# Optimization experiments

Measured on AMD Instinct MI355X. Metric: run time of the kernel, lower is better.

Reference implementation:

```python
import jax, jax.numpy as jnp
import numpy as np

NUM_EMB = 8192
DIM = 64
DECAY = 0.99
EPS = 1e-05
COMMIT = 0.25


def setup_inputs() -> dict:
    key = jax.random.key(0)
    k1, k2, k3 = jax.random.split(key, 3)
    inputs = jax.random.normal(k1, (8, 4096, DIM), jnp.float32)
    weight = jax.random.normal(k2, (NUM_EMB, DIM), jnp.float32)
    ema_cluster_count = jnp.ones((NUM_EMB,), jnp.float32)
    ema_weight_sum = jax.random.normal(k3, (NUM_EMB, DIM), jnp.float32)
    return {
        'inputs': inputs,
        'weight': weight,
        'ema_cluster_count': ema_cluster_count,
        'ema_weight_sum': ema_weight_sum,
    }


def reference(inputs, weight, ema_cluster_count, ema_weight_sum):
    flat = inputs.reshape(-1, DIM)  # [N, D]
    distances = (
        jnp.sum(flat ** 2, axis=1, keepdims=True)
        + jnp.sum(weight ** 2, axis=1)
        - 2.0 * flat @ weight.T
    )
    idx = jnp.argmin(distances, axis=1)  # [N] int

    # EMA stats (training branch): one-hot column sums == segment counts,
    # encodings.T @ flat == segment sums of inputs by code index.
    counts = jax.ops.segment_sum(
        jnp.ones(flat.shape[0], jnp.float32), idx, num_segments=NUM_EMB)
    new_cc = ema_cluster_count * DECAY + (1.0 - DECAY) * counts
    emb_sum = jax.ops.segment_sum(flat, idx, num_segments=NUM_EMB)
    new_ws = ema_weight_sum * DECAY + (1.0 - DECAY) * emb_sum

    n = jnp.sum(new_cc)
    smoothed = (new_cc + EPS) / (n + NUM_EMB * EPS) * n
    new_weight = new_ws / smoothed[:, None]  # updated codebook [K, D]

    quantized_raw = new_weight[idx].reshape(inputs.shape)
    e_latent_loss = jnp.mean((jax.lax.stop_gradient(quantized_raw) - inputs) ** 2)
    vq_loss = COMMIT * e_latent_loss

    avg_probs = counts / flat.shape[0]
    perplexity = jnp.exp(-jnp.sum(avg_probs * jnp.log(avg_probs + 1e-10)))

    # straight-through estimator
    quantized = inputs + jax.lax.stop_gradient(quantized_raw - inputs)
    return quantized, vq_loss, idx, perplexity, new_weight, new_cc, new_ws
```

## Files before the change

### kernel.cpp

```cpp
#include <hip/hip_runtime.h>
#include <math.h>

typedef _Float16 f16x8 __attribute__((ext_vector_type(8)));
typedef float f32x4 __attribute__((ext_vector_type(4)));

#define NROWS 32768
#define KEMB  8192

#define DECAYF 0.99f
#define OMDF   0.01f

#define OUT_Q    0
#define OUT_LOSS 2097152
#define OUT_IDX  2097153
#define OUT_PERP 2129921
#define OUT_NW   2129922
#define OUT_NCC  2654210
#define OUT_NWS  2662402

#define WS_N      0
#define WS_ENT    1
#define WS_COUNTS 4
#define WS_EMB    8196
#define WS_IDX    532484
#define WS_W2H    565252
#define WS_WFRAG  573444
#define WS_ZERO_UNITS 532484

__device__ __forceinline__ float sq_rn(float v) { return __fmul_rn(v, v); }

__device__ __forceinline__ float npsumsq64(const float* vbuf) {
  float a[8];
#pragma unroll
  for (int j = 0; j < 8; ++j) a[j] = sq_rn(vbuf[j]);
#pragma unroll
  for (int m = 1; m < 8; ++m)
#pragma unroll
    for (int j = 0; j < 8; ++j) a[j] = __fadd_rn(a[j], sq_rn(vbuf[m*8 + j]));
  return __fadd_rn(__fadd_rn(__fadd_rn(a[0],a[1]), __fadd_rn(a[2],a[3])),
                   __fadd_rn(__fadd_rn(a[4],a[5]), __fadd_rn(a[6],a[7])));
}

__device__ __forceinline__ void split_f16(float x, _Float16& hi, _Float16& lo) {
  hi = (_Float16)x;
  float r = __fsub_rn(x, (float)hi);
  lo = (_Float16)r;
}

__global__ __launch_bounds__(256) void prep_kernel(const float* __restrict__ wg,
                                                   float* __restrict__ ws) {
  const int tid = blockIdx.x * 256 + threadIdx.x;
  if (tid < KEMB) {
    const float* src = wg + (size_t)tid * 64;
    float vbuf[64];
#pragma unroll
    for (int f = 0; f < 16; ++f) {
      float4 v = *(const float4*)(src + f*4);
      vbuf[f*4+0]=v.x; vbuf[f*4+1]=v.y; vbuf[f*4+2]=v.z; vbuf[f*4+3]=v.w;
    }
    ws[WS_W2H + tid] = __fmul_rn(0.5f, npsumsq64(vbuf));
  } else if (tid < KEMB + 65536) {
    const int u = tid - KEMB;
    const int K = u >> 3, g = u & 7;
    const int n = K & 15, P = K >> 4;
    const int slot = (g&3)*16 + n, shi = g >> 2;
    const float* src = wg + (size_t)K*64 + g*8;
    float4 v0 = *(const float4*)src, v1 = *(const float4*)(src + 4);
    float vv[8] = {v0.x,v0.y,v0.z,v0.w,v1.x,v1.y,v1.z,v1.w};
    f16x8 hi, lo;
#pragma unroll
    for (int j = 0; j < 8; ++j) { _Float16 h, l; split_f16(vv[j], h, l); hi[j]=h; lo[j]=l; }
    _Float16* wf = (_Float16*)(ws + WS_WFRAG);
    *(f16x8*)&wf[((size_t)(P*4 + shi)*64 + slot)*8]     = hi;
    *(f16x8*)&wf[((size_t)(P*4 + 2 + shi)*64 + slot)*8] = lo;
  }
}

#define COMPUTE_PANEL(I, B0, B1, B2, B3, W2)                                        \
  {                                                                                 \
    const f32x4 cin = {(W2), (W2), (W2), (W2)};                                     \
    f32x4 acc[4];                                                                   \
    _Pragma("unroll")                                                               \
    for (int rt = 0; rt < 4; ++rt) acc[rt] = __builtin_amdgcn_mfma_f32_16x16x32_f16(a[rt][0], (B0), cin, 0,0,0); \
    _Pragma("unroll")                                                               \
    for (int rt = 0; rt < 4; ++rt) acc[rt] = __builtin_amdgcn_mfma_f32_16x16x32_f16(a[rt][1], (B1), acc[rt], 0,0,0); \
    _Pragma("unroll")                                                               \
    for (int rt = 0; rt < 4; ++rt) acc[rt] = __builtin_amdgcn_mfma_f32_16x16x32_f16(a[rt][2], (B0), acc[rt], 0,0,0); \
    _Pragma("unroll")                                                               \
    for (int rt = 0; rt < 4; ++rt) acc[rt] = __builtin_amdgcn_mfma_f32_16x16x32_f16(a[rt][3], (B1), acc[rt], 0,0,0); \
    _Pragma("unroll")                                                               \
    for (int rt = 0; rt < 4; ++rt) acc[rt] = __builtin_amdgcn_mfma_f32_16x16x32_f16(a[rt][0], (B2), acc[rt], 0,0,0); \
    _Pragma("unroll")                                                               \
    for (int rt = 0; rt < 4; ++rt) acc[rt] = __builtin_amdgcn_mfma_f32_16x16x32_f16(a[rt][1], (B3), acc[rt], 0,0,0); \
    const int kk = (I)*64 + cg*16 + n16;                                            \
    _Pragma("unroll")                                                               \
    for (int rt = 0; rt < 4; ++rt)                                                  \
      _Pragma("unroll")                                                             \
      for (int reg = 0; reg < 4; ++reg) {                                           \
        const float dist = acc[rt][reg];                                            \
        const int bi = rt*4 + reg;                                                  \
        if (dist < best[bi]) { best[bi] = dist; bestk[bi] = kk; }                   \
      }                                                                             \
  }

#define LOADB(I, C0, C1, C2, C3, CW)                                                \
  {                                                                                 \
    const size_t base = ((size_t)((I)*4 + cg) * 256) * 8 + lane8;                   \
    C0 = *(const f16x8*)&wfrag[base];                                               \
    C1 = *(const f16x8*)&wfrag[base + 512];                                         \
    C2 = *(const f16x8*)&wfrag[base + 1024];                                        \
    C3 = *(const f16x8*)&wfrag[base + 1536];                                        \
    CW = w2hg[(I)*64 + cg*16 + n16];                                                \
  }

__global__ __launch_bounds__(512) void argmin_kernel(const float* __restrict__ xg,
                                                     float* __restrict__ out,
                                                     float* __restrict__ ws) {
  __shared__ __align__(16) _Float16 xp[8*4*64*8];
  __shared__ float md[128*4];
  __shared__ int   mk[128*4];
  __shared__ int   bkL[128];

  const int t    = threadIdx.x;
  const int lane = t & 63, wv = t >> 6;
  const int quad = lane >> 4, n16 = lane & 15;
  const int rg = wv >> 2, cg = wv & 3;
  const int row0 = blockIdx.x * 128;
  const _Float16* __restrict__ wfrag = (const _Float16*)(ws + WS_WFRAG);
  const float* __restrict__ w2hg = ws + WS_W2H;

#pragma unroll
  for (int it = 0; it < 2; ++it) {
    const int u  = t + 512*it;
    const int rp = u >> 7, n = (u >> 3) & 15, g = u & 7;
    const float* src = xg + (size_t)(row0 + rp*16 + n)*64 + g*8;
    float4 v0 = *(const float4*)src, v1 = *(const float4*)(src + 4);
    float vv[8] = {v0.x,v0.y,v0.z,v0.w,v1.x,v1.y,v1.z,v1.w};
    f16x8 hi, lo;
#pragma unroll
    for (int j = 0; j < 8; ++j) { _Float16 h, l; split_f16(-vv[j], h, l); hi[j]=h; lo[j]=l; }
    const int slot = (g&3)*16 + n, shi = g >> 2;
    *(f16x8*)&xp[(((rp*4) + shi)*64 + slot)*8]     = hi;
    *(f16x8*)&xp[(((rp*4) + 2 + shi)*64 + slot)*8] = lo;
  }
  __syncthreads();

  f16x8 a[4][4];
#pragma unroll
  for (int rt = 0; rt < 4; ++rt)
#pragma unroll
    for (int s = 0; s < 4; ++s)
      a[rt][s] = *(const f16x8*)&xp[(((rg*4+rt)*4 + s)*64 + lane)*8];

  float best[16]; int bestk[16];
#pragma unroll
  for (int i = 0; i < 16; ++i) { best[i] = INFINITY; bestk[i] = 0; }

  const size_t lane8 = (size_t)lane * 8;
  f16x8 p0, p1, p2, p3, q0, q1, q2, q3;
  float pw, qw;
  LOADB(0, p0, p1, p2, p3, pw);

  for (int it = 0; it < 128; it += 2) {
    LOADB(it+1, q0, q1, q2, q3, qw);
    COMPUTE_PANEL(it, p0, p1, p2, p3, pw);
    if (it + 2 < 128) LOADB(it+2, p0, p1, p2, p3, pw);
    COMPUTE_PANEL(it+1, q0, q1, q2, q3, qw);
  }

#pragma unroll
  for (int bi = 0; bi < 16; ++bi) {
    float bd = best[bi]; int bk = bestk[bi];
#pragma unroll
    for (int m = 1; m < 16; m <<= 1) {
      const float od = __shfl_xor(bd, m, 64);
      const int   ok = __shfl_xor(bk, m, 64);
      if (od < bd || (od == bd && ok < bk)) { bd = od; bk = ok; }
    }
    best[bi] = bd; bestk[bi] = bk;
  }
  if (n16 == 0) {
#pragma unroll
    for (int rt = 0; rt < 4; ++rt)
#pragma unroll
      for (int reg = 0; reg < 4; ++reg) {
        const int row = rg*64 + rt*16 + quad*4 + reg;
        md[row*4 + cg] = best[rt*4+reg];
        mk[row*4 + cg] = bestk[rt*4+reg];
      }
  }
  __syncthreads();

  if (t < 128) {
    const int row = t;
    float bd = md[row*4]; int bk = mk[row*4];
#pragma unroll
    for (int u = 1; u < 4; ++u) {
      const float d2 = md[row*4 + u]; const int k2 = mk[row*4 + u];
      if (d2 < bd || (d2 == bd && k2 < bk)) { bd = d2; bk = k2; }
    }
    out[OUT_IDX + row0 + row] = (float)bk;
    ((int*)ws)[WS_IDX + row0 + row] = bk;
    bkL[row] = bk;
    atomicAdd(&ws[WS_COUNTS + bk], 1.0f);
  }
  __syncthreads();

#pragma unroll 4
  for (int r = 0; r < 16; ++r) {
    const int row = wv*16 + r;
    const int k = bkL[row];
    atomicAdd(&ws[WS_EMB + (size_t)k*64 + lane],
              xg[(size_t)(row0 + row)*64 + lane]);
  }
}

__global__ __launch_bounds__(256) void stats_kernel(const float* __restrict__ cc,
                                                    float* __restrict__ out,
                                                    float* __restrict__ ws) {
  const int t = threadIdx.x;
  float v1 = 0.0f, v2 = 0.0f;
#pragma unroll
  for (int i = 0; i < 32; ++i) {
    const int k = i*256 + t;
    const float cnt = ws[WS_COUNTS + k];
    const float ncc = __fadd_rn(__fmul_rn(DECAYF, cc[k]), __fmul_rn(OMDF, cnt));
    out[OUT_NCC + k] = ncc;
    const float p = cnt * (1.0f/32768.0f);
    v1 += ncc;
    v2 += __fmul_rn(p, logf(__fadd_rn(p, 1e-10f)));
  }
#pragma unroll
  for (int off = 32; off > 0; off >>= 1) {
    v1 += __shfl_down(v1, off);
    v2 += __shfl_down(v2, off);
  }
  __shared__ float s1[4], s2[4];
  const int lane = t & 63, wid = t >> 6;
  if (lane == 0) { s1[wid] = v1; s2[wid] = v2; }
  __syncthreads();
  if (t == 0) {
    ws[WS_N]   = (s1[0]+s1[1]) + (s1[2]+s1[3]);
    ws[WS_ENT] = (s2[0]+s2[1]) + (s2[2]+s2[3]);
  }
}

__global__ __launch_bounds__(256) void update_kernel(const float* __restrict__ ws0,
                                                     float* __restrict__ out,
                                                     float* __restrict__ ws) {
  const int e4 = blockIdx.x * 256 + threadIdx.x;
  const int k = e4 >> 4;
  const float n = ws[WS_N];
  const float ncc = out[OUT_NCC + k];
  const float smoothed = __fmul_rn(__fadd_rn(ncc, 1e-5f) / __fadd_rn(n, 0.08192f), n);
  const float inv_s = 1.0f / smoothed;
  float4 w0 = *(const float4*)(ws0 + (size_t)e4*4);
  float4 em = *(const float4*)(ws + WS_EMB + (size_t)e4*4);
  float wv[4] = {w0.x, w0.y, w0.z, w0.w};
  float ev[4] = {em.x, em.y, em.z, em.w};
  float nwsv[4], nwv[4];
#pragma unroll
  for (int i = 0; i < 4; ++i) {
    nwsv[i] = __fadd_rn(__fmul_rn(DECAYF, wv[i]), __fmul_rn(OMDF, ev[i]));
    nwv[i]  = nwsv[i] / smoothed;
  }
  (void)inv_s;
  float4 onws = {nwsv[0], nwsv[1], nwsv[2], nwsv[3]};
  float4 onw  = {nwv[0],  nwv[1],  nwv[2],  nwv[3]};
  *(float4*)(out + OUT_NWS + (size_t)e4*4) = onws;
  *(float4*)(out + OUT_NW  + (size_t)e4*4) = onw;
  if (e4 == 0) out[OUT_PERP] = expf(-ws[WS_ENT]);
}

__global__ __launch_bounds__(256) void quant_kernel(const float* __restrict__ xg,
                                                    float* __restrict__ out,
                                                    float* __restrict__ ws) {
  const int t = threadIdx.x;
  const int* idxb = (const int*)ws + WS_IDX;
  float v = 0.0f;
#pragma unroll
  for (int j = 0; j < 4; ++j) {
    const int e4 = (j*512 + blockIdx.x)*256 + t;
    const int row = e4 >> 4, d = (e4 & 15) * 4;
    const int k = idxb[row];
    const float* nw = out + OUT_NW + (size_t)k*64 + d;
    float2 q0 = *(const float2*)nw, q1 = *(const float2*)(nw + 2);
    float4 x = *(const float4*)(xg + (size_t)e4*4);
    float qv[4] = {q0.x, q0.y, q1.x, q1.y};
    float xv[4] = {x.x, x.y, x.z, x.w};
    float4 o;
    float ov[4];
#pragma unroll
    for (int i = 0; i < 4; ++i) {
      const float df = __fsub_rn(qv[i], xv[i]);
      ov[i] = __fadd_rn(xv[i], df);
      v = fmaf(df, df, v);
    }
    o.x = ov[0]; o.y = ov[1]; o.z = ov[2]; o.w = ov[3];
    *(float4*)(out + OUT_Q + (size_t)e4*4) = o;
  }
#pragma unroll
  for (int off = 32; off > 0; off >>= 1) v += __shfl_down(v, off);
  __shared__ float sm[4];
  const int lane = t & 63, wid = t >> 6;
  if (lane == 0) sm[wid] = v;
  __syncthreads();
  if (t == 0) ws[WS_COUNTS + blockIdx.x] = (sm[0]+sm[1]) + (sm[2]+sm[3]);
}

__global__ void final_kernel(float* __restrict__ out, const float* __restrict__ ws) {
  const int t = threadIdx.x;
  float v = 0.0f;
#pragma unroll
  for (int i = 0; i < 8; ++i) v += ws[WS_COUNTS + i*64 + t];
#pragma unroll
  for (int off = 32; off > 0; off >>= 1) v += __shfl_down(v, off);
  if (t == 0) out[OUT_LOSS] = __fmul_rn(0.25f, v / 2097152.0f);
}

extern "C" void kernel_launch(void* const* d_in, const int* in_sizes, int n_in,
                              void* d_out, int out_size, void* d_ws, size_t ws_size,
                              hipStream_t stream) {
  (void)in_sizes; (void)n_in; (void)out_size; (void)ws_size;
  const float* x   = (const float*)d_in[0];
  const float* w   = (const float*)d_in[1];
  const float* cc  = (const float*)d_in[2];
  const float* ws0 = (const float*)d_in[3];
  float* out = (float*)d_out;
  float* ws  = (float*)d_ws;

  hipMemsetAsync(d_ws, 0, (size_t)WS_ZERO_UNITS * 4, stream);
  hipLaunchKernelGGL(prep_kernel,   dim3(288),  dim3(256), 0, stream, w, ws);
  hipLaunchKernelGGL(argmin_kernel, dim3(256),  dim3(512), 0, stream, x, out, ws);
  hipLaunchKernelGGL(stats_kernel,  dim3(1),    dim3(256), 0, stream, cc, out, ws);
  hipLaunchKernelGGL(update_kernel, dim3(512),  dim3(256), 0, stream, ws0, out, ws);
  hipLaunchKernelGGL(quant_kernel,  dim3(512),  dim3(256), 0, stream, x, out, ws);
  hipLaunchKernelGGL(final_kernel,  dim3(1),    dim3(64),  0, stream, out, ws);
}
```

Measured before the change: 186.3 us.

## Restructure argmin MFMA with swapped operands, 1024-thread blocks, fuse update into quant

The argmin kernel now uses 16 waves per block, each owning a strip of codebook columns. MFMA operands are swapped so codebook fragments are the A operand and input rows stay resident in registers as B. The loop is single-buffered with setprio hints and takes a per-lane min over 4 accumulator values, so the per-row cross-lane reduction shrinks. Separately, the update and quantize kernels are merged into one, and the gathered quantized values are recomputed from ws0 and the embedding sums instead of being read back from new_weight. This removes a launch and a dependency but does redundant division work per element.

```diff
diff --git a/kernel.cpp b/kernel.cpp
--- a/kernel.cpp
+++ b/kernel.cpp
@@ -76,62 +76,24 @@
   }
 }
 
-#define COMPUTE_PANEL(I, B0, B1, B2, B3, W2)                                        \
-  {                                                                                 \
-    const f32x4 cin = {(W2), (W2), (W2), (W2)};                                     \
-    f32x4 acc[4];                                                                   \
-    _Pragma("unroll")                                                               \
-    for (int rt = 0; rt < 4; ++rt) acc[rt] = __builtin_amdgcn_mfma_f32_16x16x32_f16(a[rt][0], (B0), cin, 0,0,0); \
-    _Pragma("unroll")                                                               \
-    for (int rt = 0; rt < 4; ++rt) acc[rt] = __builtin_amdgcn_mfma_f32_16x16x32_f16(a[rt][1], (B1), acc[rt], 0,0,0); \
-    _Pragma("unroll")                                                               \
-    for (int rt = 0; rt < 4; ++rt) acc[rt] = __builtin_amdgcn_mfma_f32_16x16x32_f16(a[rt][2], (B0), acc[rt], 0,0,0); \
-    _Pragma("unroll")                                                               \
-    for (int rt = 0; rt < 4; ++rt) acc[rt] = __builtin_amdgcn_mfma_f32_16x16x32_f16(a[rt][3], (B1), acc[rt], 0,0,0); \
-    _Pragma("unroll")                                                               \
-    for (int rt = 0; rt < 4; ++rt) acc[rt] = __builtin_amdgcn_mfma_f32_16x16x32_f16(a[rt][0], (B2), acc[rt], 0,0,0); \
-    _Pragma("unroll")                                                               \
-    for (int rt = 0; rt < 4; ++rt) acc[rt] = __builtin_amdgcn_mfma_f32_16x16x32_f16(a[rt][1], (B3), acc[rt], 0,0,0); \
-    const int kk = (I)*64 + cg*16 + n16;                                            \
-    _Pragma("unroll")                                                               \
-    for (int rt = 0; rt < 4; ++rt)                                                  \
-      _Pragma("unroll")                                                             \
-      for (int reg = 0; reg < 4; ++reg) {                                           \
-        const float dist = acc[rt][reg];                                            \
-        const int bi = rt*4 + reg;                                                  \
-        if (dist < best[bi]) { best[bi] = dist; bestk[bi] = kk; }                   \
-      }                                                                             \
-  }
-
-#define LOADB(I, C0, C1, C2, C3, CW)                                                \
-  {                                                                                 \
-    const size_t base = ((size_t)((I)*4 + cg) * 256) * 8 + lane8;                   \
-    C0 = *(const f16x8*)&wfrag[base];                                               \
-    C1 = *(const f16x8*)&wfrag[base + 512];                                         \
-    C2 = *(const f16x8*)&wfrag[base + 1024];                                        \
-    C3 = *(const f16x8*)&wfrag[base + 1536];                                        \
-    CW = w2hg[(I)*64 + cg*16 + n16];                                                \
-  }
-
-__global__ __launch_bounds__(512) void argmin_kernel(const float* __restrict__ xg,
-                                                     float* __restrict__ out,
-                                                     float* __restrict__ ws) {
+__global__ __launch_bounds__(1024) void argmin_kernel(const float* __restrict__ xg,
+                                                      float* __restrict__ out,
+                                                      float* __restrict__ ws) {
   __shared__ __align__(16) _Float16 xp[8*4*64*8];
-  __shared__ float md[128*4];
-  __shared__ int   mk[128*4];
+  __shared__ float md[128*8];
+  __shared__ int   mk[128*8];
   __shared__ int   bkL[128];
 
   const int t    = threadIdx.x;
   const int lane = t & 63, wv = t >> 6;
   const int quad = lane >> 4, n16 = lane & 15;
-  const int rg = wv >> 2, cg = wv & 3;
+  const int rg = wv >> 3, cg = wv & 7;
   const int row0 = blockIdx.x * 128;
   const _Float16* __restrict__ wfrag = (const _Float16*)(ws + WS_WFRAG);
   const float* __restrict__ w2hg = ws + WS_W2H;
 
-#pragma unroll
-  for (int it = 0; it < 2; ++it) {
-    const int u  = t + 512*it;
+  {
+    const int u  = t;
     const int rp = u >> 7, n = (u >> 3) & 15, g = u & 7;
     const float* src = xg + (size_t)(row0 + rp*16 + n)*64 + g*8;
     float4 v0 = *(const float4*)src, v1 = *(const float4*)(src + 4);
@@ -145,58 +107,97 @@
   }
   __syncthreads();
 
-  f16x8 a[4][4];
-#pragma unroll
-  for (int rt = 0; rt < 4; ++rt)
+  f16x8 b[4][4];
+#pragma unroll
+  for (int bt = 0; bt < 4; ++bt)
 #pragma unroll
     for (int s = 0; s < 4; ++s)
-      a[rt][s] = *(const f16x8*)&xp[(((rg*4+rt)*4 + s)*64 + lane)*8];
-
-  float best[16]; int bestk[16];
-#pragma unroll
-  for (int i = 0; i < 16; ++i) { best[i] = INFINITY; bestk[i] = 0; }
+      b[bt][s] = *(const f16x8*)&xp[(((rg*4+bt)*4 + s)*64 + lane)*8];
+
+  float bestd[4]; int bestk[4];
+#pragma unroll
+  for (int i = 0; i < 4; ++i) { bestd[i] = INFINITY; bestk[i] = 0; }
 
   const size_t lane8 = (size_t)lane * 8;
-  f16x8 p0, p1, p2, p3, q0, q1, q2, q3;
-  float pw, qw;
-  LOADB(0, p0, p1, p2, p3, pw);
-
-  for (int it = 0; it < 128; it += 2) {
-    LOADB(it+1, q0, q1, q2, q3, qw);
-    COMPUTE_PANEL(it, p0, p1, p2, p3, pw);
-    if (it + 2 < 128) LOADB(it+2, p0, p1, p2, p3, pw);
-    COMPUTE_PANEL(it+1, q0, q1, q2, q3, qw);
-  }
-
-#pragma unroll
-  for (int bi = 0; bi < 16; ++bi) {
-    float bd = best[bi]; int bk = bestk[bi];
-#pragma unroll
-    for (int m = 1; m < 16; m <<= 1) {
+  const int q4 = quad * 4;
+
+  f16x8 wh0, wh1, wl0, wl1;
+  int kb = cg;
+  {
+    const size_t base = (size_t)kb * 2048 + lane8;
+    wh0 = *(const f16x8*)&wfrag[base];
+    wh1 = *(const f16x8*)&wfrag[base + 512];
+    wl0 = *(const f16x8*)&wfrag[base + 1024];
+    wl1 = *(const f16x8*)&wfrag[base + 1536];
+  }
+  float4 cw = *(const float4*)&w2hg[kb*16 + q4];
+
+#pragma unroll 1
+  for (int it = 0; it < 64; ++it) {
+    const f32x4 cin = {cw.x, cw.y, cw.z, cw.w};
+    const int c0 = kb*16 + q4;
+    f32x4 acc[4];
+    __builtin_amdgcn_s_setprio(1);
+#pragma unroll
+    for (int bt = 0; bt < 4; ++bt) acc[bt] = __builtin_amdgcn_mfma_f32_16x16x32_f16(wh0, b[bt][0], cin,     0,0,0);
+#pragma unroll
+    for (int bt = 0; bt < 4; ++bt) acc[bt] = __builtin_amdgcn_mfma_f32_16x16x32_f16(wh1, b[bt][1], acc[bt], 0,0,0);
+#pragma unroll
+    for (int bt = 0; bt < 4; ++bt) acc[bt] = __builtin_amdgcn_mfma_f32_16x16x32_f16(wh0, b[bt][2], acc[bt], 0,0,0);
+#pragma unroll
+    for (int bt = 0; bt < 4; ++bt) acc[bt] = __builtin_amdgcn_mfma_f32_16x16x32_f16(wh1, b[bt][3], acc[bt], 0,0,0);
+#pragma unroll
+    for (int bt = 0; bt < 4; ++bt) acc[bt] = __builtin_amdgcn_mfma_f32_16x16x32_f16(wl0, b[bt][0], acc[bt], 0,0,0);
+#pragma unroll
+    for (int bt = 0; bt < 4; ++bt) acc[bt] = __builtin_amdgcn_mfma_f32_16x16x32_f16(wl1, b[bt][1], acc[bt], 0,0,0);
+    __builtin_amdgcn_s_setprio(0);
+
+    if (it < 63) {
+      const int pn = kb + 8;
+      const size_t base = (size_t)pn * 2048 + lane8;
+      wh0 = *(const f16x8*)&wfrag[base];
+      wh1 = *(const f16x8*)&wfrag[base + 512];
+      wl0 = *(const f16x8*)&wfrag[base + 1024];
+      wl1 = *(const f16x8*)&wfrag[base + 1536];
+      cw  = *(const float4*)&w2hg[pn*16 + q4];
+      kb = pn;
+    }
+
+#pragma unroll
+    for (int bt = 0; bt < 4; ++bt) {
+      const float d0 = acc[bt][0], d1 = acc[bt][1], d2 = acc[bt][2], d3 = acc[bt][3];
+      const float pm = fminf(fminf(d0, d1), fminf(d2, d3));
+      int koff = 3;
+      if (d2 == pm) koff = 2;
+      if (d1 == pm) koff = 1;
+      if (d0 == pm) koff = 0;
+      if (pm < bestd[bt]) { bestd[bt] = pm; bestk[bt] = c0 + koff; }
+    }
+  }
+
+#pragma unroll
+  for (int bt = 0; bt < 4; ++bt) {
+    float bd = bestd[bt]; int bk = bestk[bt];
+#pragma unroll
+    for (int m = 16; m < 64; m <<= 1) {
       const float od = __shfl_xor(bd, m, 64);
       const int   ok = __shfl_xor(bk, m, 64);
       if (od < bd || (od == bd && ok < bk)) { bd = od; bk = ok; }
     }
-    best[bi] = bd; bestk[bi] = bk;
-  }
-  if (n16 == 0) {
-#pragma unroll
-    for (int rt = 0; rt < 4; ++rt)
-#pragma unroll
-      for (int reg = 0; reg < 4; ++reg) {
-        const int row = rg*64 + rt*16 + quad*4 + reg;
-        md[row*4 + cg] = best[rt*4+reg];
-        mk[row*4 + cg] = bestk[rt*4+reg];
-      }
+    if (lane < 16) {
+      const int row = rg*64 + bt*16 + n16;
+      md[row*8 + cg] = bd;
+      mk[row*8 + cg] = bk;
+    }
   }
   __syncthreads();
 
   if (t < 128) {
     const int row = t;
-    float bd = md[row*4]; int bk = mk[row*4];
-#pragma unroll
-    for (int u = 1; u < 4; ++u) {
-      const float d2 = md[row*4 + u]; const int k2 = mk[row*4 + u];
+    float bd = md[row*8]; int bk = mk[row*8];
+#pragma unroll
+    for (int u2 = 1; u2 < 8; ++u2) {
+      const float d2 = md[row*8 + u2]; const int k2 = mk[row*8 + u2];
       if (d2 < bd || (d2 == bd && k2 < bk)) { bd = d2; bk = k2; }
     }
     out[OUT_IDX + row0 + row] = (float)bk;
@@ -206,9 +207,9 @@
   }
   __syncthreads();
 
-#pragma unroll 4
-  for (int r = 0; r < 16; ++r) {
-    const int row = wv*16 + r;
+#pragma unroll
+  for (int r = 0; r < 8; ++r) {
+    const int row = wv*8 + r;
     const int k = bkL[row];
     atomicAdd(&ws[WS_EMB + (size_t)k*64 + lane],
               xg[(size_t)(row0 + row)*64 + lane]);
@@ -245,59 +246,62 @@
   }
 }
 
-__global__ __launch_bounds__(256) void update_kernel(const float* __restrict__ ws0,
-                                                     float* __restrict__ out,
-                                                     float* __restrict__ ws) {
-  const int e4 = blockIdx.x * 256 + threadIdx.x;
-  const int k = e4 >> 4;
+__global__ __launch_bounds__(256) void update_quant_kernel(const float* __restrict__ xg,
+                                                           const float* __restrict__ ws0,
+                                                           float* __restrict__ out,
+                                                           float* __restrict__ ws) {
+  const int t = threadIdx.x;
   const float n = ws[WS_N];
-  const float ncc = out[OUT_NCC + k];
-  const float smoothed = __fmul_rn(__fadd_rn(ncc, 1e-5f) / __fadd_rn(n, 0.08192f), n);
-  const float inv_s = 1.0f / smoothed;
-  float4 w0 = *(const float4*)(ws0 + (size_t)e4*4);
-  float4 em = *(const float4*)(ws + WS_EMB + (size_t)e4*4);
-  float wv[4] = {w0.x, w0.y, w0.z, w0.w};
-  float ev[4] = {em.x, em.y, em.z, em.w};
-  float nwsv[4], nwv[4];
-#pragma unroll
-  for (int i = 0; i < 4; ++i) {
-    nwsv[i] = __fadd_rn(__fmul_rn(DECAYF, wv[i]), __fmul_rn(OMDF, ev[i]));
-    nwv[i]  = nwsv[i] / smoothed;
-  }
-  (void)inv_s;
-  float4 onws = {nwsv[0], nwsv[1], nwsv[2], nwsv[3]};
-  float4 onw  = {nwv[0],  nwv[1],  nwv[2],  nwv[3]};
-  *(float4*)(out + OUT_NWS + (size_t)e4*4) = onws;
-  *(float4*)(out + OUT_NW  + (size_t)e4*4) = onw;
-  if (e4 == 0) out[OUT_PERP] = expf(-ws[WS_ENT]);
-}
-
-__global__ __launch_bounds__(256) void quant_kernel(const float* __restrict__ xg,
-                                                    float* __restrict__ out,
-                                                    float* __restrict__ ws) {
-  const int t = threadIdx.x;
+  const float den = __fadd_rn(n, 0.08192f);
+
+  const int e4 = blockIdx.x * 256 + t;
+  {
+    const int k = e4 >> 4;
+    const float ncc = out[OUT_NCC + k];
+    const float smoothed = __fmul_rn(__fadd_rn(ncc, 1e-5f) / den, n);
+    float4 w0 = *(const float4*)(ws0 + (size_t)e4*4);
+    float4 em = *(const float4*)(ws + WS_EMB + (size_t)e4*4);
+    float wv4[4] = {w0.x, w0.y, w0.z, w0.w};
+    float ev4[4] = {em.x, em.y, em.z, em.w};
+    float nwsv[4], nwv[4];
+#pragma unroll
+    for (int i = 0; i < 4; ++i) {
+      nwsv[i] = __fadd_rn(__fmul_rn(DECAYF, wv4[i]), __fmul_rn(OMDF, ev4[i]));
+      nwv[i]  = nwsv[i] / smoothed;
+    }
+    float4 onws = {nwsv[0], nwsv[1], nwsv[2], nwsv[3]};
+    float4 onw  = {nwv[0],  nwv[1],  nwv[2],  nwv[3]};
+    *(float4*)(out + OUT_NWS + (size_t)e4*4) = onws;
+    *(float4*)(out + OUT_NW  + (size_t)e4*4) = onw;
+    if (e4 == 0) out[OUT_PERP] = expf(-ws[WS_ENT]);
+  }
+
   const int* idxb = (const int*)ws + WS_IDX;
   float v = 0.0f;
 #pragma unroll
   for (int j = 0; j < 4; ++j) {
-    const int e4 = (j*512 + blockIdx.x)*256 + t;
-    const int row = e4 >> 4, d = (e4 & 15) * 4;
+    const int qe4 = (j*512 + blockIdx.x)*256 + t;
+    const int row = qe4 >> 4, d = (qe4 & 15) * 4;
     const int k = idxb[row];
-    const float* nw = out + OUT_NW + (size_t)k*64 + d;
-    float2 q0 = *(const float2*)nw, q1 = *(const float2*)(nw + 2);
-    float4 x = *(const float4*)(xg + (size_t)e4*4);
-    float qv[4] = {q0.x, q0.y, q1.x, q1.y};
-    float xv[4] = {x.x, x.y, x.z, x.w};
-    float4 o;
-    float ov[4];
+    const float ncc = out[OUT_NCC + k];
+    const float smK = __fmul_rn(__fadd_rn(ncc, 1e-5f) / den, n);
+    float4 wq = *(const float4*)(ws0 + (size_t)k*64 + d);
+    float4 eq = *(const float4*)(ws + WS_EMB + (size_t)k*64 + d);
+    float4 x  = *(const float4*)(xg + (size_t)qe4*4);
+    float wv4[4] = {wq.x,wq.y,wq.z,wq.w};
+    float ev4[4] = {eq.x,eq.y,eq.z,eq.w};
+    float xv[4]  = {x.x,x.y,x.z,x.w};
+    float4 o; float ov[4];
 #pragma unroll
     for (int i = 0; i < 4; ++i) {
-      const float df = __fsub_rn(qv[i], xv[i]);
+      const float nws = __fadd_rn(__fmul_rn(DECAYF, wv4[i]), __fmul_rn(OMDF, ev4[i]));
+      const float q = nws / smK;
+      const float df = __fsub_rn(q, xv[i]);
       ov[i] = __fadd_rn(xv[i], df);
       v = fmaf(df, df, v);
     }
     o.x = ov[0]; o.y = ov[1]; o.z = ov[2]; o.w = ov[3];
-    *(float4*)(out + OUT_Q + (size_t)e4*4) = o;
+    *(float4*)(out + OUT_Q + (size_t)qe4*4) = o;
   }
 #pragma unroll
   for (int off = 32; off > 0; off >>= 1) v += __shfl_down(v, off);
@@ -330,10 +334,9 @@
   float* ws  = (float*)d_ws;
 
   hipMemsetAsync(d_ws, 0, (size_t)WS_ZERO_UNITS * 4, stream);
-  hipLaunchKernelGGL(prep_kernel,   dim3(288),  dim3(256), 0, stream, w, ws);
-  hipLaunchKernelGGL(argmin_kernel, dim3(256),  dim3(512), 0, stream, x, out, ws);
-  hipLaunchKernelGGL(stats_kernel,  dim3(1),    dim3(256), 0, stream, cc, out, ws);
-  hipLaunchKernelGGL(update_kernel, dim3(512),  dim3(256), 0, stream, ws0, out, ws);
-  hipLaunchKernelGGL(quant_kernel,  dim3(512),  dim3(256), 0, stream, x, out, ws);
-  hipLaunchKernelGGL(final_kernel,  dim3(1),    dim3(64),  0, stream, out, ws);
-}
+  hipLaunchKernelGGL(prep_kernel,         dim3(288), dim3(256),  0, stream, w, ws);
+  hipLaunchKernelGGL(argmin_kernel,       dim3(256), dim3(1024), 0, stream, x, out, ws);
+  hipLaunchKernelGGL(stats_kernel,        dim3(1),   dim3(256),  0, stream, cc, out, ws);
+  hipLaunchKernelGGL(update_quant_kernel, dim3(512), dim3(256),  0, stream, x, ws0, out, ws);
+  hipLaunchKernelGGL(final_kernel,        dim3(1),   dim3(64),   0, stream, out, ws);
+}
```

After: 181.0 us. -2.8%, faster.
